# Performance work log

Measured on AMD Instinct MI355X. Metric: run time of the kernel, lower is better.

Reference implementation:

```python
import jax, jax.numpy as jnp
import numpy as np

B, S, D = 1, 2048, 2048
NH, NKV, HD = 32, 8, 64
EPS = 1e-5
SCALE = float(HD) ** 0.5


def _rope(x, cos, sin):
    # x: [b, h, s, hd]; cos/sin: [s, hd//2]; interleaved-pair rotary (executorch style)
    xr = x[..., 0::2]
    xi = x[..., 1::2]
    c = cos[None, None, :, :]
    s = sin[None, None, :, :]
    out_r = xr * c - xi * s
    out_i = xr * s + xi * c
    return jnp.stack([out_r, out_i], axis=-1).reshape(x.shape)


def _rmsnorm(x, w):
    var = jnp.mean(x * x, axis=-1, keepdims=True)
    return x * jax.lax.rsqrt(var + EPS) * w


def setup_inputs() -> dict:
    key = jax.random.key(0)
    ks = jax.random.split(key, 6)
    hidden_states = jax.random.normal(ks[0], (B, S, D), dtype=jnp.float32)
    # standard Llama rope tables, theta=10000
    inv_freq = 1.0 / (10000.0 ** (np.arange(0, HD, 2, dtype=np.float32) / HD))
    t = np.arange(S, dtype=np.float32)
    ang = np.outer(t, inv_freq)  # [S, HD//2]
    freqs_cos = jnp.asarray(np.cos(ang), dtype=jnp.float32)
    freqs_sin = jnp.asarray(np.sin(ang), dtype=jnp.float32)
    # additive causal mask [1,1,S,S]
    causal = jnp.tril(jnp.ones((S, S), dtype=bool))
    atten_mask = jnp.where(causal, 0.0, -1e9).astype(jnp.float32)[None, None]
    sd = 1.0 / np.sqrt(D)
    wq = jax.random.normal(ks[1], (NH * HD, D), dtype=jnp.float32) * sd
    wk = jax.random.normal(ks[2], (NKV * HD, D), dtype=jnp.float32) * sd
    wv = jax.random.normal(ks[3], (NKV * HD, D), dtype=jnp.float32) * sd
    wo = jax.random.normal(ks[4], (D, NH * HD), dtype=jnp.float32) * sd
    q_norm_w = jnp.ones((HD,), dtype=jnp.float32)
    k_norm_w = jnp.ones((HD,), dtype=jnp.float32)
    return dict(hidden_states=hidden_states, freqs_cos=freqs_cos, freqs_sin=freqs_sin,
                atten_mask=atten_mask, wq=wq, wk=wk, wv=wv, wo=wo,
                q_norm_w=q_norm_w, k_norm_w=k_norm_w)


def reference(hidden_states, freqs_cos, freqs_sin, atten_mask, wq, wk, wv, wo, q_norm_w, k_norm_w):
    b, s, _ = hidden_states.shape
    n_rep = NH // NKV
    # fused QKV projections (Linear: x @ W.T)
    q = (hidden_states @ wq.T).reshape(b, s, NH, HD).transpose(0, 2, 1, 3)   # [b,nh,s,hd]
    k = (hidden_states @ wk.T).reshape(b, s, NKV, HD).transpose(0, 2, 1, 3)  # [b,nkv,s,hd]
    v = (hidden_states @ wv.T).reshape(b, s, NKV, HD).transpose(0, 2, 1, 3)
    # RoPE, then QK RMSNorm (qk_norm_before_rope=False)
    q = _rope(q, freqs_cos, freqs_sin)
    k = _rope(k, freqs_cos, freqs_sin)
    q = _rmsnorm(q, q_norm_w)
    k = _rmsnorm(k, k_norm_w)
    # no KV cache (prefill): kh = k^T, vh = v, then GQA repeat
    kh = jnp.repeat(k, n_rep, axis=1)  # [b,nh,s,hd]
    vh = jnp.repeat(v, n_rep, axis=1)
    attn = jnp.einsum('bhqd,bhkd->bhqk', q, kh) / SCALE
    attn = jax.nn.softmax(attn + atten_mask, axis=-1)
    y = jnp.einsum('bhqk,bhkd->bhqd', attn, vh)
    y = y.transpose(0, 2, 1, 3).reshape(b, s, NH * HD)
    y = y @ wo.T
    # module returns (y, [kh], [vh]); kh stored transposed (b,nh,hd,s)
    return (y, kh.transpose(0, 1, 3, 2), vh)
```

## Files before the change

kernel.cpp:

```cpp
#include <hip/hip_runtime.h>
#include <cstdint>
#include <cstddef>

#define S_   2048
#define D_   2048
#define NH_  32
#define NKV_ 8
#define HD_  64

using bf16x8 = __attribute__((ext_vector_type(8))) __bf16;
using f32x4  = __attribute__((ext_vector_type(4))) float;

#define AS_GLOBAL(p) (const __attribute__((address_space(1))) void*)(p)
#define AS_LDS(p)    (__attribute__((address_space(3))) void*)(p)

__device__ __forceinline__ float b2f(uint u) {
  union { uint u; float f; } c; c.u = u << 16; return c.f;
}

__global__ __launch_bounds__(256) void cvt_all(
    const float* __restrict__ hs, const float* __restrict__ wq,
    const float* __restrict__ wk, const float* __restrict__ wv,
    const float* __restrict__ wo,
    __bf16* __restrict__ hs_bf, __bf16* __restrict__ wq_bf,
    __bf16* __restrict__ wk_bf, __bf16* __restrict__ wv_bf,
    __bf16* __restrict__ wo_bf) {
  int i = blockIdx.x * 256 + threadIdx.x;
  const float* src; __bf16* dst; int base;
  if (i < 1048576)      { src = hs; dst = hs_bf; base = 0; }
  else if (i < 2097152) { src = wq; dst = wq_bf; base = 1048576; }
  else if (i < 2359296) { src = wk; dst = wk_bf; base = 2097152; }
  else if (i < 2621440) { src = wv; dst = wv_bf; base = 2359296; }
  else                  { src = wo; dst = wo_bf; base = 2621440; }
  i -= base;
  const float4 v = reinterpret_cast<const float4*>(src)[i];
  __bf16 t[4] = {(__bf16)v.x, (__bf16)v.y, (__bf16)v.z, (__bf16)v.w};
  reinterpret_cast<uint2*>(dst)[i] = *reinterpret_cast<uint2*>(t);
}

__device__ __forceinline__ void gemm_compute_step(
    const char* ldsA, const char* ldsB, f32x4 (&acc)[4][4],
    int l15, int lg, int wm, int wn) {
  bf16x8 af[4][2], bfr[4][2];
#pragma unroll
  for (int f = 0; f < 4; ++f) {
    const int arow = wm*64 + f*16 + l15;
    const int brow = wn*64 + f*16 + l15;
#pragma unroll
    for (int ks = 0; ks < 2; ++ks) {
      af[f][ks] = *reinterpret_cast<const bf16x8*>(
          ldsA + arow*128 + (((ks*4 + lg) ^ (arow & 7)) << 4));
      bfr[f][ks] = *reinterpret_cast<const bf16x8*>(
          ldsB + brow*128 + (((ks*4 + lg) ^ (brow & 7)) << 4));
    }
  }
#pragma unroll
  for (int mf = 0; mf < 4; ++mf)
#pragma unroll
    for (int nf = 0; nf < 4; ++nf) {
      acc[mf][nf] = __builtin_amdgcn_mfma_f32_16x16x32_bf16(
          af[mf][0], bfr[nf][0], acc[mf][nf], 0, 0, 0);
      acc[mf][nf] = __builtin_amdgcn_mfma_f32_16x16x32_bf16(
          af[mf][1], bfr[nf][1], acc[mf][nf], 0, 0, 0);
    }
}

__device__ __forceinline__ void gemm_tile_128_bf(
    const __bf16* __restrict__ A, const __bf16* __restrict__ B,
    __bf16* __restrict__ C, int K, int N, int m0, int n0) {
  __shared__ __align__(16) char lds[2][32768];
  const int tid = threadIdx.x;
  const int l = tid & 63;
  const int w = tid >> 6;
  const int l15 = l & 15, lg = l >> 4;
  const int wm = w >> 1, wn = w & 1;

  f32x4 acc[4][4] = {};

  const int srow   = tid >> 3;
  const int schunk = (tid & 7) ^ (srow & 7);
  const __bf16* gA = A + (size_t)(m0 + srow) * K + schunk * 8;
  const __bf16* gB = B + (size_t)(n0 + srow) * K + schunk * 8;
  const int ldst = tid * 16;
  const int nt = K >> 6;

#pragma unroll
  for (int i = 0; i < 4; ++i) {
    __builtin_amdgcn_global_load_lds(AS_GLOBAL(gA + (size_t)i*32*K),
                                     AS_LDS(&lds[0][i*4096 + ldst]), 16, 0, 0);
    __builtin_amdgcn_global_load_lds(AS_GLOBAL(gB + (size_t)i*32*K),
                                     AS_LDS(&lds[0][16384 + i*4096 + ldst]), 16, 0, 0);
  }
  __syncthreads();

  int cur = 0;
  for (int t = 0; t < nt; ++t) {
    if (t + 1 < nt) {
      const int k0 = (t + 1) * 64;
      char* dA = &lds[cur ^ 1][0];
      char* dB = &lds[cur ^ 1][16384];
#pragma unroll
      for (int i = 0; i < 4; ++i) {
        __builtin_amdgcn_global_load_lds(AS_GLOBAL(gA + (size_t)i*32*K + k0),
                                         AS_LDS(dA + i*4096 + ldst), 16, 0, 0);
        __builtin_amdgcn_global_load_lds(AS_GLOBAL(gB + (size_t)i*32*K + k0),
                                         AS_LDS(dB + i*4096 + ldst), 16, 0, 0);
      }
    }
    gemm_compute_step(&lds[cur][0], &lds[cur][16384], acc, l15, lg, wm, wn);
    __syncthreads();
    cur ^= 1;
  }

#pragma unroll
  for (int mf = 0; mf < 4; ++mf)
#pragma unroll
    for (int nf = 0; nf < 4; ++nf)
#pragma unroll
      for (int r = 0; r < 4; ++r)
        C[(size_t)(m0 + wm*64 + mf*16 + lg*4 + r) * N + n0 + wn*64 + nf*16 + l15]
            = (__bf16)acc[mf][nf][r];
}

__device__ __forceinline__ void gemm_tile_128_d2(
    const __bf16* __restrict__ A, const __bf16* __restrict__ B,
    float* __restrict__ C, int K, int N, int m0, int n0) {
  __shared__ __align__(16) char lds[3][32768];
  const int tid = threadIdx.x;
  const int l = tid & 63;
  const int w = tid >> 6;
  const int l15 = l & 15, lg = l >> 4;
  const int wm = w >> 1, wn = w & 1;

  f32x4 acc[4][4] = {};

  const int srow   = tid >> 3;
  const int schunk = (tid & 7) ^ (srow & 7);
  const __bf16* gA = A + (size_t)(m0 + srow) * K + schunk * 8;
  const __bf16* gB = B + (size_t)(n0 + srow) * K + schunk * 8;
  const int ldst = tid * 16;
  const int nt = K >> 6;

#pragma unroll
  for (int i = 0; i < 4; ++i) {
    __builtin_amdgcn_global_load_lds(AS_GLOBAL(gA + (size_t)i*32*K),
                                     AS_LDS(&lds[0][i*4096 + ldst]), 16, 0, 0);
    __builtin_amdgcn_global_load_lds(AS_GLOBAL(gB + (size_t)i*32*K),
                                     AS_LDS(&lds[0][16384 + i*4096 + ldst]), 16, 0, 0);
  }
#pragma unroll
  for (int i = 0; i < 4; ++i) {
    __builtin_amdgcn_global_load_lds(AS_GLOBAL(gA + (size_t)i*32*K + 64),
                                     AS_LDS(&lds[1][i*4096 + ldst]), 16, 0, 0);
    __builtin_amdgcn_global_load_lds(AS_GLOBAL(gB + (size_t)i*32*K + 64),
                                     AS_LDS(&lds[1][16384 + i*4096 + ldst]), 16, 0, 0);
  }

  char* p0 = &lds[0][0];
  char* p1 = &lds[1][0];
  char* p2 = &lds[2][0];

  for (int t = 0; t < nt; ++t) {
    if (t + 1 < nt) asm volatile("s_waitcnt vmcnt(8)" ::: "memory");
    else            asm volatile("s_waitcnt vmcnt(0)" ::: "memory");
    __builtin_amdgcn_s_barrier();

    if (t + 2 < nt) {
      const int k0 = (t + 2) * 64;
#pragma unroll
      for (int i = 0; i < 4; ++i) {
        __builtin_amdgcn_global_load_lds(AS_GLOBAL(gA + (size_t)i*32*K + k0),
                                         AS_LDS(p2 + i*4096 + ldst), 16, 0, 0);
        __builtin_amdgcn_global_load_lds(AS_GLOBAL(gB + (size_t)i*32*K + k0),
                                         AS_LDS(p2 + 16384 + i*4096 + ldst), 16, 0, 0);
      }
    }

    gemm_compute_step(p0, p0 + 16384, acc, l15, lg, wm, wn);

    char* tmp = p0; p0 = p1; p1 = p2; p2 = tmp;
  }

#pragma unroll
  for (int mf = 0; mf < 4; ++mf)
#pragma unroll
    for (int nf = 0; nf < 4; ++nf)
#pragma unroll
      for (int r = 0; r < 4; ++r)
        C[(size_t)(m0 + wm*64 + mf*16 + lg*4 + r) * N + n0 + wn*64 + nf*16 + l15]
            = acc[mf][nf][r];
}

__global__ __launch_bounds__(256) void gemm_qkv(
    const __bf16* __restrict__ hs,
    const __bf16* __restrict__ wq, const __bf16* __restrict__ wk,
    const __bf16* __restrict__ wv,
    __bf16* __restrict__ qp, __bf16* __restrict__ kp, __bf16* __restrict__ vp) {
  const int bx = blockIdx.x;
  const __bf16* Bm; __bf16* Cm; int N, n0;
  if (bx < 16)      { Bm = wq; Cm = qp; N = 2048; n0 = bx * 128; }
  else if (bx < 20) { Bm = wk; Cm = kp; N = 512;  n0 = (bx - 16) * 128; }
  else              { Bm = wv; Cm = vp; N = 512;  n0 = (bx - 20) * 128; }
  gemm_tile_128_bf(hs, Bm, Cm, 2048, N, blockIdx.y * 128, n0);
}

__global__ __launch_bounds__(256) void gemm_wo(
    const __bf16* __restrict__ ypre, const __bf16* __restrict__ wo,
    float* __restrict__ y) {
  gemm_tile_128_d2(ypre, wo, y, 2048, 2048, blockIdx.y * 128, blockIdx.x * 128);
}

__global__ __launch_bounds__(256) void rope_norm_qk(
    const __bf16* __restrict__ qp, const __bf16* __restrict__ kp,
    const float* __restrict__ cosT, const float* __restrict__ sinT,
    const float* __restrict__ qw, const float* __restrict__ kw,
    __bf16* __restrict__ qbf, __bf16* __restrict__ kbf) {
  const int wid_all = (int)((blockIdx.x * 256 + threadIdx.x) >> 6);
  const int lane = threadIdx.x & 63;
  if (wid_all < 65536) {
    const int s = wid_all >> 5;
    const int hh = wid_all & 31;
    const size_t idx = (size_t)s*D_ + hh*HD_ + lane;
    float val = (float)qp[idx];
    const float c  = cosT[s*32 + (lane >> 1)];
    const float sn = sinT[s*32 + (lane >> 1)];
    const float partner = __shfl_xor(val, 1);
    const float ro = (lane & 1) ? fmaf(partner, sn, val*c)
                                : fmaf(val, c, -partner*sn);
    float ssq = ro * ro;
#pragma unroll
    for (int off = 32; off >= 1; off >>= 1) ssq += __shfl_xor(ssq, off);
    const float rinv = rsqrtf(ssq * (1.0f/64.0f) + 1e-5f);
    qbf[idx] = (__bf16)(ro * rinv * qw[lane] * 0.180336880111120426f);
  } else {
    const int wid = wid_all - 65536;
    const int s   = wid >> 3;
    const int kvh = wid & 7;
    const size_t idx = (size_t)s*(NKV_*HD_) + kvh*HD_ + lane;
    float val = (float)kp[idx];
    const float c  = cosT[s*32 + (lane >> 1)];
    const float sn = sinT[s*32 + (lane >> 1)];
    const float partner = __shfl_xor(val, 1);
    const float ro = (lane & 1) ? fmaf(partner, sn, val*c)
                                : fmaf(val, c, -partner*sn);
    float ssq = ro * ro;
#pragma unroll
    for (int off = 32; off >= 1; off >>= 1) ssq += __shfl_xor(ssq, off);
    const float rinv = rsqrtf(ssq * (1.0f/64.0f) + 1e-5f);
    kbf[idx] = (__bf16)(ro * rinv * kw[lane]);
  }
}

__global__ __launch_bounds__(256) void transpose_kv(
    const __bf16* __restrict__ kpost, float* __restrict__ khT,
    const __bf16* __restrict__ vp, float* __restrict__ vh,
    __bf16* __restrict__ vtbf) {
  __shared__ float tl[64][68];
  const int kvh = blockIdx.y;
  const int t = threadIdx.x;
  if (blockIdx.x < 32) {
    const int s0 = blockIdx.x * 64;
    {
      const int d0 = (t & 15) * 4;
      const int sl = t >> 4;
#pragma unroll
      for (int rep = 0; rep < 4; ++rep) {
        const int srow = sl + rep*16;
        const uint2 v = *reinterpret_cast<const uint2*>(
            &kpost[(size_t)(s0 + srow)*(NKV_*HD_) + kvh*HD_ + d0]);
        tl[d0+0][srow] = b2f(v.x & 0xffff);
        tl[d0+1][srow] = b2f(v.x >> 16);
        tl[d0+2][srow] = b2f(v.y & 0xffff);
        tl[d0+3][srow] = b2f(v.y >> 16);
      }
    }
    __syncthreads();
    {
      const int d  = t >> 2;
      const int s4 = (t & 3) * 16;
#pragma unroll
      for (int c = 0; c < 4; ++c) {
        float4 v;
        v.x = tl[d][s4+c*4+0]; v.y = tl[d][s4+c*4+1];
        v.z = tl[d][s4+c*4+2]; v.w = tl[d][s4+c*4+3];
#pragma unroll
        for (int r = 0; r < 4; ++r) {
          *reinterpret_cast<float4*>(
              &khT[((size_t)(kvh*4 + r)*HD_ + d)*S_ + s0 + s4 + c*4]) = v;
        }
      }
    }
  } else {
    const int s0 = (blockIdx.x - 32) * 64;
    const int srow = t >> 2, dc = (t & 3) * 16;
    const __bf16* src = &vp[(size_t)(s0 + srow)*(NKV_*HD_) + kvh*HD_ + dc];
    const uint4 a = reinterpret_cast<const uint4*>(src)[0];
    const uint4 b = reinterpret_cast<const uint4*>(src)[1];
    float f[16];
    f[0]=b2f(a.x&0xffff); f[1]=b2f(a.x>>16); f[2]=b2f(a.y&0xffff); f[3]=b2f(a.y>>16);
    f[4]=b2f(a.z&0xffff); f[5]=b2f(a.z>>16); f[6]=b2f(a.w&0xffff); f[7]=b2f(a.w>>16);
    f[8]=b2f(b.x&0xffff); f[9]=b2f(b.x>>16); f[10]=b2f(b.y&0xffff); f[11]=b2f(b.y>>16);
    f[12]=b2f(b.z&0xffff); f[13]=b2f(b.z>>16); f[14]=b2f(b.w&0xffff); f[15]=b2f(b.w>>16);
#pragma unroll
    for (int i = 0; i < 16; ++i) tl[srow][dc + i] = f[i];
#pragma unroll
    for (int r = 0; r < 4; ++r) {
      float* dst = &vh[((size_t)(kvh*4 + r)*S_ + s0 + srow)*HD_ + dc];
#pragma unroll
      for (int cc = 0; cc < 4; ++cc) {
        float4 v4 = {f[cc*4+0], f[cc*4+1], f[cc*4+2], f[cc*4+3]};
        reinterpret_cast<float4*>(dst)[cc] = v4;
      }
    }
    __syncthreads();
    const int dr = t >> 2, sc = (t & 3) * 16;
    __bf16 vals[16];
#pragma unroll
    for (int i = 0; i < 16; ++i) vals[i] = (__bf16)tl[sc + i][dr];
    uint4* dst = reinterpret_cast<uint4*>(&vtbf[((size_t)(kvh*64 + dr))*S_ + s0 + sc]);
    dst[0] = reinterpret_cast<uint4*>(vals)[0];
    dst[1] = reinterpret_cast<uint4*>(vals)[1];
  }
}

__device__ __forceinline__ uint pack2bf(float a, float b) {
  __bf16 x = (__bf16)a, y = (__bf16)b;
  const uint ux = (uint)*reinterpret_cast<ushort*>(&x);
  const uint uy = (uint)*reinterpret_cast<ushort*>(&y);
  return ux | (uy << 16);
}

__device__ __forceinline__ void qk_tile_T(
    const char* kldh, bf16x8 qf0, bf16x8 qf1, f32x4 (&s_)[4],
    int l15, int lg) {
  __builtin_amdgcn_s_setprio(1);
#pragma unroll
  for (int nb = 0; nb < 4; ++nb) {
    const int row = nb*16 + l15;
    const int bc  = lg*16;
    const bf16x8 kb0 = *reinterpret_cast<const bf16x8*>(
        kldh + row*128 + ((bc)      ^ ((row & 7) << 4)));
    const bf16x8 kb1 = *reinterpret_cast<const bf16x8*>(
        kldh + row*128 + ((bc + 64) ^ ((row & 7) << 4)));
    f32x4 t = f32x4{0.f, 0.f, 0.f, 0.f};
    t = __builtin_amdgcn_mfma_f32_16x16x32_bf16(kb0, qf0, t, 0, 0, 0);
    t = __builtin_amdgcn_mfma_f32_16x16x32_bf16(kb1, qf1, t, 0, 0, 0);
    s_[nb] = t;
  }
  __builtin_amdgcn_s_setprio(0);
}

__device__ __forceinline__ void softmax_pv_T(
    f32x4 (&s_)[4], float& m_, float& l_, f32x4 (&o_)[4],
    char* pldw, const char* vbase, int l15, int lg) {
  float mx = fmaxf(fmaxf(s_[0][0], s_[0][1]), fmaxf(s_[0][2], s_[0][3]));
#pragma unroll
  for (int nb = 1; nb < 4; ++nb) {
    mx = fmaxf(mx, fmaxf(fmaxf(s_[nb][0], s_[nb][1]),
                         fmaxf(s_[nb][2], s_[nb][3])));
  }
  mx = fmaxf(mx, __shfl_xor(mx, 16));
  mx = fmaxf(mx, __shfl_xor(mx, 32));
  const float mnew = fmaxf(m_, mx);
  const float scl = exp2f(m_ - mnew);
  m_ = mnew;

  const int swz = (l15 & 7) << 4;
  float ls = 0.f;
#pragma unroll
  for (int nb = 0; nb < 4; ++nb) {
    float p0 = exp2f(s_[nb][0] - mnew);
    float p1 = exp2f(s_[nb][1] - mnew);
    float p2 = exp2f(s_[nb][2] - mnew);
    float p3 = exp2f(s_[nb][3] - mnew);
    ls += (p0 + p1) + (p2 + p3);
    *reinterpret_cast<uint*>(pldw + ((l15*128 + nb*32 + lg*8)     ^ swz)) = pack2bf(p0, p1);
    *reinterpret_cast<uint*>(pldw + ((l15*128 + nb*32 + lg*8 + 4) ^ swz)) = pack2bf(p2, p3);
  }
  ls += __shfl_xor(ls, 16);
  ls += __shfl_xor(ls, 32);
  l_ = l_*scl + ls;
#pragma unroll
  for (int nb = 0; nb < 4; ++nb) {
    o_[nb][0] *= scl; o_[nb][1] *= scl; o_[nb][2] *= scl; o_[nb][3] *= scl;
  }

  const bf16x8 pb0 = *reinterpret_cast<const bf16x8*>(
      pldw + ((l15*128 + lg*16)      ^ swz));
  const bf16x8 pb1 = *reinterpret_cast<const bf16x8*>(
      pldw + ((l15*128 + lg*16 + 64) ^ swz));

  __builtin_amdgcn_s_setprio(1);
#pragma unroll
  for (int nb = 0; nb < 4; ++nb) {
    const int row = nb*16 + l15;
    const int bc  = lg*16;
    const bf16x8 v0 = *reinterpret_cast<const bf16x8*>(
        vbase + row*128 + ((bc)      ^ ((row & 7) << 4)));
    const bf16x8 v1 = *reinterpret_cast<const bf16x8*>(
        vbase + row*128 + ((bc + 64) ^ ((row & 7) << 4)));
    f32x4 t = o_[nb];
    t = __builtin_amdgcn_mfma_f32_16x16x32_bf16(v0, pb0, t, 0, 0, 0);
    t = __builtin_amdgcn_mfma_f32_16x16x32_bf16(v1, pb1, t, 0, 0, 0);
    o_[nb] = t;
  }
  __builtin_amdgcn_s_setprio(0);
}

__device__ __forceinline__ void mask_diag_T(f32x4 (&s_)[4], int l15, int lg, int wg) {
  const int qrow = wg*16 + l15;
#pragma unroll
  for (int nb = 0; nb < 4; ++nb)
#pragma unroll
    for (int r = 0; r < 4; ++r)
      if (nb*16 + lg*4 + r > qrow) s_[nb][r] = -1e30f;
}

__global__ __launch_bounds__(512, 4) void flash_attn_mfma(
    const __bf16* __restrict__ qbf, const __bf16* __restrict__ kbf,
    const __bf16* __restrict__ vtbf, __bf16* __restrict__ ypre) {
  __shared__ __align__(16) char smem[49152];

  const int h   = blockIdx.y;
  const int pi  = blockIdx.x;
  const int qbA = pi, qbB = 31 - pi;
  const int SS  = (qbB >> 1) + 1;
  const int kvh = h >> 2;
  const int tid = threadIdx.x;
  const int l   = tid & 63;
  const int w   = tid >> 6;
  const int g   = tid >> 8;
  const int wg  = w & 3;
  const int l15 = l & 15;
  const int lg  = l >> 4;

  char* kldg = smem + g*8192;
  char* vtlg = smem + 16384 + g*8192;
  char* pldw = smem + 32768 + w*2048;

  const int ts = tid & 255;
  const int j  = ts >> 2;
  const int c0 = (ts & 3) * 16;
  const int b0 = (j*128 + c0*2)      ^ ((j & 7) << 4);
  const int b1 = (j*128 + c0*2 + 16) ^ ((j & 7) << 4);
  const __bf16* ksrc = kbf  + (size_t)(g*64 + j)*(NKV_*HD_) + kvh*HD_ + c0;
  const __bf16* vsrc = vtbf + (size_t)(kvh*64 + j)*S_ + g*64 + c0;

  bf16x8 qfA0, qfA1, qfB0, qfB1;
  {
    const __bf16* qa = qbf + (size_t)(qbA*64 + wg*16 + l15)*D_ + h*HD_ + lg*8;
    qfA0 = *reinterpret_cast<const bf16x8*>(qa);
    qfA1 = *reinterpret_cast<const bf16x8*>(qa + 32);
    const __bf16* qb = qbf + (size_t)(qbB*64 + wg*16 + l15)*D_ + h*HD_ + lg*8;
    qfB0 = *reinterpret_cast<const bf16x8*>(qb);
    qfB1 = *reinterpret_cast<const bf16x8*>(qb + 32);
  }

  f32x4 oA[4], oB[4];
#pragma unroll
  for (int nb = 0; nb < 4; ++nb) {
    oA[nb] = f32x4{0.f, 0.f, 0.f, 0.f};
    oB[nb] = f32x4{0.f, 0.f, 0.f, 0.f};
  }
  float mA = -1e30f, lA = 0.f, mB = -1e30f, lB = 0.f;

  uint4 kr0 = reinterpret_cast<const uint4*>(ksrc)[0];
  uint4 kr1 = reinterpret_cast<const uint4*>(ksrc + 8)[0];
  uint4 vr0 = reinterpret_cast<const uint4*>(vsrc)[0];
  uint4 vr1 = reinterpret_cast<const uint4*>(vsrc + 8)[0];

  for (int st = 0; st < SS; ++st) {
    __syncthreads();
    *reinterpret_cast<uint4*>(kldg + b0) = kr0;
    *reinterpret_cast<uint4*>(kldg + b1) = kr1;
    *reinterpret_cast<uint4*>(vtlg + b0) = vr0;
    *reinterpret_cast<uint4*>(vtlg + b1) = vr1;
    __syncthreads();

    if (st + 1 < SS) {
      const __bf16* kn = ksrc + (size_t)(st + 1)*128*(NKV_*HD_);
      const __bf16* vn = vsrc + (size_t)(st + 1)*128;
      kr0 = reinterpret_cast<const uint4*>(kn)[0];
      kr1 = reinterpret_cast<const uint4*>(kn + 8)[0];
      vr0 = reinterpret_cast<const uint4*>(vn)[0];
      vr1 = reinterpret_cast<const uint4*>(vn + 8)[0];
    }

    const int kt = 2*st + g;
    if (kt <= qbB) {
      f32x4 s_[4];
      qk_tile_T(kldg, qfB0, qfB1, s_, l15, lg);
      if (kt == qbB) mask_diag_T(s_, l15, lg, wg);
      softmax_pv_T(s_, mB, lB, oB, pldw, vtlg, l15, lg);
    }
    if (kt <= qbA) {
      f32x4 s_[4];
      qk_tile_T(kldg, qfA0, qfA1, s_, l15, lg);
      if (kt == qbA) mask_diag_T(s_, l15, lg, wg);
      softmax_pv_T(s_, mA, lA, oA, pldw, vtlg, l15, lg);
    }
  }

  float* ox = reinterpret_cast<float*>(smem);
  float* ml = reinterpret_cast<float*>(smem + 20480);
  float* po = ox + (wg*64 + l)*17;
  float* pm = ml + (wg*64 + l)*9;

  __syncthreads();
  if (g == 1) {
#pragma unroll
    for (int nb = 0; nb < 4; ++nb)
#pragma unroll
      for (int r = 0; r < 4; ++r) po[nb*4 + r] = oB[nb][r];
    pm[0] = mB; pm[1] = lB;
  }
  __syncthreads();
  if (g == 0) {
    const float m1 = pm[0], l1 = pm[1];
    const float m = fmaxf(mB, m1);
    const float s0 = exp2f(mB - m), s1 = exp2f(m1 - m);
    lB = lB*s0 + l1*s1;
#pragma unroll
    for (int nb = 0; nb < 4; ++nb)
#pragma unroll
      for (int r = 0; r < 4; ++r)
        oB[nb][r] = oB[nb][r]*s0 + po[nb*4 + r]*s1;
  }
  __syncthreads();
  if (g == 1) {
#pragma unroll
    for (int nb = 0; nb < 4; ++nb)
#pragma unroll
      for (int r = 0; r < 4; ++r) po[nb*4 + r] = oA[nb][r];
    pm[0] = mA; pm[1] = lA;
  }
  __syncthreads();
  if (g == 0) {
    const float m1 = pm[0], l1 = pm[1];
    const float m = fmaxf(mA, m1);
    const float s0 = exp2f(mA - m), s1 = exp2f(m1 - m);
    lA = lA*s0 + l1*s1;
#pragma unroll
    for (int nb = 0; nb < 4; ++nb)
#pragma unroll
      for (int r = 0; r < 4; ++r)
        oA[nb][r] = oA[nb][r]*s0 + po[nb*4 + r]*s1;

    const float rlA = 1.0f / lA, rlB = 1.0f / lB;
    const size_t rowA = (size_t)(qbA*64 + wg*16 + l15)*D_ + h*HD_;
    const size_t rowB = (size_t)(qbB*64 + wg*16 + l15)*D_ + h*HD_;
#pragma unroll
    for (int nb = 0; nb < 4; ++nb) {
      uint2 pa, pb;
      pa.x = pack2bf(oA[nb][0]*rlA, oA[nb][1]*rlA);
      pa.y = pack2bf(oA[nb][2]*rlA, oA[nb][3]*rlA);
      pb.x = pack2bf(oB[nb][0]*rlB, oB[nb][1]*rlB);
      pb.y = pack2bf(oB[nb][2]*rlB, oB[nb][3]*rlB);
      *reinterpret_cast<uint2*>(&ypre[rowA + nb*16 + lg*4]) = pa;
      *reinterpret_cast<uint2*>(&ypre[rowB + nb*16 + lg*4]) = pb;
    }
  }
}

extern "C" void kernel_launch(void* const* d_in, const int* in_sizes, int n_in,
                              void* d_out, int out_size, void* d_ws, size_t ws_size,
                              hipStream_t stream) {
  (void)in_sizes; (void)n_in; (void)out_size;
  const float* hs   = (const float*)d_in[0];
  const float* fcos = (const float*)d_in[1];
  const float* fsin = (const float*)d_in[2];
  const float* wq = (const float*)d_in[4];
  const float* wk = (const float*)d_in[5];
  const float* wv = (const float*)d_in[6];
  const float* wo = (const float*)d_in[7];
  const float* qw = (const float*)d_in[8];
  const float* kw = (const float*)d_in[9];

  float* out = (float*)d_out;
  float* y   = out;
  float* khT = out + 4194304;
  float* vh  = out + 8388608;

  __bf16* qbf   = (__bf16*)y;
  __bf16* kbf   = (__bf16*)((char*)y + 8*1024*1024);
  __bf16* vtbf  = (__bf16*)((char*)y + 10*1024*1024);
  __bf16* hs_bf = (__bf16*)khT;
  __bf16* wq_bf = (__bf16*)((char*)khT + 8*1024*1024);
  __bf16* wk_bf = (__bf16*)vh;
  __bf16* wv_bf = (__bf16*)((char*)vh + 2*1024*1024);

  const size_t need = (size_t)40 * 1024 * 1024;
  if (ws_size < need) return;
  char* ws = (char*)d_ws;
  __bf16* qp_bf   = (__bf16*)(ws);
  __bf16* kp_bf   = (__bf16*)(ws + 8*1024*1024);
  __bf16* vp_bf   = (__bf16*)(ws + 10*1024*1024);
  __bf16* ypre_bf = (__bf16*)(ws + 12*1024*1024);
  __bf16* wo_bf   = (__bf16*)(ws + 20*1024*1024);

  cvt_all<<<14336, 256, 0, stream>>>(hs, wq, wk, wv, wo,
                                     hs_bf, wq_bf, wk_bf, wv_bf, wo_bf);

  gemm_qkv<<<dim3(24, 16), 256, 0, stream>>>(hs_bf, wq_bf, wk_bf, wv_bf,
                                             qp_bf, kp_bf, vp_bf);

  rope_norm_qk<<<20480, 256, 0, stream>>>(qp_bf, kp_bf, fcos, fsin, qw, kw,
                                          qbf, kbf);

  transpose_kv<<<dim3(64, 8), 256, 0, stream>>>(kbf, khT, vp_bf, vh, vtbf);

  flash_attn_mfma<<<dim3(16, 32), 512, 0, stream>>>(qbf, kbf, vtbf, ypre_bf);

  gemm_wo<<<dim3(16, 16), 256, 0, stream>>>(ypre_bf, wo_bf, y);
}
```

Before: 147.3 us.

## Fuse RoPE and QK RMSNorm into QKV GEMM epilogue; lazy softmax rescale

Moves the rotary embedding and RMSNorm for Q and K into the QKV projection GEMM epilogue, so the GEMM writes normalized bf16 Q/K directly and the separate rope_norm_qk kernel and its intermediate buffers go away. This removes one launch and a full read/write of the Q/K projections. In the flash attention softmax, the running max is now only updated, with O and l rescaled, when some lane's new max exceeds the old one by more than 8 in log2 space. The lazy rescale saves work on most tiles but lets the exp values grow up to 2^8, which puts some pressure on bf16 precision for P.

```diff
diff --git a/kernel.cpp b/kernel.cpp
--- a/kernel.cpp
+++ b/kernel.cpp
@@ -65,10 +65,13 @@
     }
 }
 
+template <int MODE>
 __device__ __forceinline__ void gemm_tile_128_bf(
+    char (*lds)[32768],
     const __bf16* __restrict__ A, const __bf16* __restrict__ B,
-    __bf16* __restrict__ C, int K, int N, int m0, int n0) {
-  __shared__ __align__(16) char lds[2][32768];
+    __bf16* __restrict__ C, int K, int N, int m0, int n0,
+    const float* __restrict__ cosT, const float* __restrict__ sinT,
+    const float* __restrict__ nw) {
   const int tid = threadIdx.x;
   const int l = tid & 63;
   const int w = tid >> 6;
@@ -112,14 +115,50 @@
     cur ^= 1;
   }
 
-#pragma unroll
-  for (int mf = 0; mf < 4; ++mf)
-#pragma unroll
-    for (int nf = 0; nf < 4; ++nf)
-#pragma unroll
-      for (int r = 0; r < 4; ++r)
-        C[(size_t)(m0 + wm*64 + mf*16 + lg*4 + r) * N + n0 + wn*64 + nf*16 + l15]
-            = (__bf16)acc[mf][nf][r];
+  if (MODE == 0) {
+#pragma unroll
+    for (int mf = 0; mf < 4; ++mf)
+#pragma unroll
+      for (int nf = 0; nf < 4; ++nf)
+#pragma unroll
+        for (int r = 0; r < 4; ++r)
+          C[(size_t)(m0 + wm*64 + mf*16 + lg*4 + r) * N + n0 + wn*64 + nf*16 + l15]
+              = (__bf16)acc[mf][nf][r];
+  } else {
+    const float fin = (MODE == 1) ? 0.180336880111120426f : 1.0f;
+    float wv_[4];
+#pragma unroll
+    for (int nf = 0; nf < 4; ++nf) wv_[nf] = nw[nf*16 + l15];
+    const int odd = l15 & 1;
+#pragma unroll
+    for (int mf = 0; mf < 4; ++mf) {
+#pragma unroll
+      for (int r = 0; r < 4; ++r) {
+        const int row = m0 + wm*64 + mf*16 + lg*4 + r;
+        float ro[4];
+        float ssq = 0.f;
+#pragma unroll
+        for (int nf = 0; nf < 4; ++nf) {
+          const float v = acc[mf][nf][r];
+          const float p = __shfl_xor(v, 1);
+          const int d2 = (nf*16 + l15) >> 1;
+          const float c  = cosT[row*32 + d2];
+          const float sn = sinT[row*32 + d2];
+          ro[nf] = odd ? fmaf(p, sn, v*c) : fmaf(v, c, -p*sn);
+          ssq = fmaf(ro[nf], ro[nf], ssq);
+        }
+        ssq += __shfl_xor(ssq, 1);
+        ssq += __shfl_xor(ssq, 2);
+        ssq += __shfl_xor(ssq, 4);
+        ssq += __shfl_xor(ssq, 8);
+        const float rinv = rsqrtf(ssq * (1.0f/64.0f) + 1e-5f);
+#pragma unroll
+        for (int nf = 0; nf < 4; ++nf)
+          C[(size_t)row * N + n0 + wn*64 + nf*16 + l15]
+              = (__bf16)(ro[nf] * rinv * wv_[nf] * fin);
+      }
+    }
+  }
 }
 
 __device__ __forceinline__ void gemm_tile_128_d2(
@@ -195,60 +234,26 @@
     const __bf16* __restrict__ hs,
     const __bf16* __restrict__ wq, const __bf16* __restrict__ wk,
     const __bf16* __restrict__ wv,
-    __bf16* __restrict__ qp, __bf16* __restrict__ kp, __bf16* __restrict__ vp) {
+    __bf16* __restrict__ qbf, __bf16* __restrict__ kbf, __bf16* __restrict__ vp,
+    const float* __restrict__ fcos, const float* __restrict__ fsin,
+    const float* __restrict__ qw, const float* __restrict__ kw) {
+  __shared__ __align__(16) char lds[2][32768];
   const int bx = blockIdx.x;
-  const __bf16* Bm; __bf16* Cm; int N, n0;
-  if (bx < 16)      { Bm = wq; Cm = qp; N = 2048; n0 = bx * 128; }
-  else if (bx < 20) { Bm = wk; Cm = kp; N = 512;  n0 = (bx - 16) * 128; }
-  else              { Bm = wv; Cm = vp; N = 512;  n0 = (bx - 20) * 128; }
-  gemm_tile_128_bf(hs, Bm, Cm, 2048, N, blockIdx.y * 128, n0);
+  const int m0 = blockIdx.y * 128;
+  if (bx < 16) {
+    gemm_tile_128_bf<1>(lds, hs, wq, qbf, 2048, 2048, m0, bx*128, fcos, fsin, qw);
+  } else if (bx < 20) {
+    gemm_tile_128_bf<2>(lds, hs, wk, kbf, 2048, 512, m0, (bx-16)*128, fcos, fsin, kw);
+  } else {
+    gemm_tile_128_bf<0>(lds, hs, wv, vp, 2048, 512, m0, (bx-20)*128,
+                        nullptr, nullptr, nullptr);
+  }
 }
 
 __global__ __launch_bounds__(256) void gemm_wo(
     const __bf16* __restrict__ ypre, const __bf16* __restrict__ wo,
     float* __restrict__ y) {
   gemm_tile_128_d2(ypre, wo, y, 2048, 2048, blockIdx.y * 128, blockIdx.x * 128);
-}
-
-__global__ __launch_bounds__(256) void rope_norm_qk(
-    const __bf16* __restrict__ qp, const __bf16* __restrict__ kp,
-    const float* __restrict__ cosT, const float* __restrict__ sinT,
-    const float* __restrict__ qw, const float* __restrict__ kw,
-    __bf16* __restrict__ qbf, __bf16* __restrict__ kbf) {
-  const int wid_all = (int)((blockIdx.x * 256 + threadIdx.x) >> 6);
-  const int lane = threadIdx.x & 63;
-  if (wid_all < 65536) {
-    const int s = wid_all >> 5;
-    const int hh = wid_all & 31;
-    const size_t idx = (size_t)s*D_ + hh*HD_ + lane;
-    float val = (float)qp[idx];
-    const float c  = cosT[s*32 + (lane >> 1)];
-    const float sn = sinT[s*32 + (lane >> 1)];
-    const float partner = __shfl_xor(val, 1);
-    const float ro = (lane & 1) ? fmaf(partner, sn, val*c)
-                                : fmaf(val, c, -partner*sn);
-    float ssq = ro * ro;
-#pragma unroll
-    for (int off = 32; off >= 1; off >>= 1) ssq += __shfl_xor(ssq, off);
-    const float rinv = rsqrtf(ssq * (1.0f/64.0f) + 1e-5f);
-    qbf[idx] = (__bf16)(ro * rinv * qw[lane] * 0.180336880111120426f);
-  } else {
-    const int wid = wid_all - 65536;
-    const int s   = wid >> 3;
-    const int kvh = wid & 7;
-    const size_t idx = (size_t)s*(NKV_*HD_) + kvh*HD_ + lane;
-    float val = (float)kp[idx];
-    const float c  = cosT[s*32 + (lane >> 1)];
-    const float sn = sinT[s*32 + (lane >> 1)];
-    const float partner = __shfl_xor(val, 1);
-    const float ro = (lane & 1) ? fmaf(partner, sn, val*c)
-                                : fmaf(val, c, -partner*sn);
-    float ssq = ro * ro;
-#pragma unroll
-    for (int off = 32; off >= 1; off >>= 1) ssq += __shfl_xor(ssq, off);
-    const float rinv = rsqrtf(ssq * (1.0f/64.0f) + 1e-5f);
-    kbf[idx] = (__bf16)(ro * rinv * kw[lane]);
-  }
 }
 
 __global__ __launch_bounds__(256) void transpose_kv(
@@ -361,29 +366,33 @@
   }
   mx = fmaxf(mx, __shfl_xor(mx, 16));
   mx = fmaxf(mx, __shfl_xor(mx, 32));
-  const float mnew = fmaxf(m_, mx);
-  const float scl = exp2f(m_ - mnew);
-  m_ = mnew;
+
+  if (!__all(mx <= m_ + 8.f)) {
+    const float mnew = fmaxf(m_, mx);
+    const float scl = exp2f(m_ - mnew);
+    m_ = mnew;
+    l_ *= scl;
+#pragma unroll
+    for (int nb = 0; nb < 4; ++nb) {
+      o_[nb][0] *= scl; o_[nb][1] *= scl; o_[nb][2] *= scl; o_[nb][3] *= scl;
+    }
+  }
 
   const int swz = (l15 & 7) << 4;
   float ls = 0.f;
 #pragma unroll
   for (int nb = 0; nb < 4; ++nb) {
-    float p0 = exp2f(s_[nb][0] - mnew);
-    float p1 = exp2f(s_[nb][1] - mnew);
-    float p2 = exp2f(s_[nb][2] - mnew);
-    float p3 = exp2f(s_[nb][3] - mnew);
+    float p0 = exp2f(s_[nb][0] - m_);
+    float p1 = exp2f(s_[nb][1] - m_);
+    float p2 = exp2f(s_[nb][2] - m_);
+    float p3 = exp2f(s_[nb][3] - m_);
     ls += (p0 + p1) + (p2 + p3);
     *reinterpret_cast<uint*>(pldw + ((l15*128 + nb*32 + lg*8)     ^ swz)) = pack2bf(p0, p1);
     *reinterpret_cast<uint*>(pldw + ((l15*128 + nb*32 + lg*8 + 4) ^ swz)) = pack2bf(p2, p3);
   }
   ls += __shfl_xor(ls, 16);
   ls += __shfl_xor(ls, 32);
-  l_ = l_*scl + ls;
-#pragma unroll
-  for (int nb = 0; nb < 4; ++nb) {
-    o_[nb][0] *= scl; o_[nb][1] *= scl; o_[nb][2] *= scl; o_[nb][3] *= scl;
-  }
+  l_ += ls;
 
   const bf16x8 pb0 = *reinterpret_cast<const bf16x8*>(
       pldw + ((l15*128 + lg*16)      ^ swz));
@@ -592,20 +601,16 @@
   const size_t need = (size_t)40 * 1024 * 1024;
   if (ws_size < need) return;
   char* ws = (char*)d_ws;
-  __bf16* qp_bf   = (__bf16*)(ws);
-  __bf16* kp_bf   = (__bf16*)(ws + 8*1024*1024);
-  __bf16* vp_bf   = (__bf16*)(ws + 10*1024*1024);
-  __bf16* ypre_bf = (__bf16*)(ws + 12*1024*1024);
-  __bf16* wo_bf   = (__bf16*)(ws + 20*1024*1024);
+  __bf16* vp_bf   = (__bf16*)(ws);
+  __bf16* ypre_bf = (__bf16*)(ws + 2*1024*1024);
+  __bf16* wo_bf   = (__bf16*)(ws + 10*1024*1024);
 
   cvt_all<<<14336, 256, 0, stream>>>(hs, wq, wk, wv, wo,
                                      hs_bf, wq_bf, wk_bf, wv_bf, wo_bf);
 
   gemm_qkv<<<dim3(24, 16), 256, 0, stream>>>(hs_bf, wq_bf, wk_bf, wv_bf,
-                                             qp_bf, kp_bf, vp_bf);
-
-  rope_norm_qk<<<20480, 256, 0, stream>>>(qp_bf, kp_bf, fcos, fsin, qw, kw,
-                                          qbf, kbf);
+                                             qbf, kbf, vp_bf,
+                                             fcos, fsin, qw, kw);
 
   transpose_kv<<<dim3(64, 8), 256, 0, stream>>>(kbf, khT, vp_bf, vh, vtbf);
 
```

New measurement: 139.7 us. 5.1% less time.
